# Kernel optimization log

Hardware: AMD Instinct MI355X
Metric: run time of the kernel (lower is better)

Reference implementation:

```python
import jax, jax.numpy as jnp
import numpy as np

C = 256  # channels
B, H, W = 16, 64, 64


def _conv1x1(x, w, b):
    # x: [B,Cin,H,W], w: [Cout,Cin], b: [Cout] -> [B,Cout,H,W]
    return jnp.einsum('bchw,oc->bohw', x, w) + b[None, :, None, None]


def _axis_attn(x, wq, bq, wf, bf, axis):
    # axis: -1 for 'W', -2 for 'H'
    qkv = _conv1x1(x, wq, bq)                      # [B,1+2C,H,W]
    query = qkv[:, :1]                             # [B,1,H,W]
    key = qkv[:, 1:1 + C]                          # [B,C,H,W]
    value = qkv[:, 1 + C:]                         # [B,C,H,W]
    scores = jax.nn.softmax(query, axis=axis)      # softmax over spatial axis
    context = jnp.sum(key * scores, axis=axis, keepdims=True)  # [B,C,H,1] or [B,C,1,W]
    gate = jax.nn.sigmoid(value)
    out = x + gate * context                       # broadcast over reduced axis
    return _conv1x1(out, wf, bf)


def setup_inputs() -> dict:
    key = jax.random.key(0)
    ks = jax.random.split(key, 5)
    s_qkv = 1.0 / np.sqrt(C)
    s_fus = 1.0 / np.sqrt(C)
    return {
        'x': jax.random.normal(ks[0], (B, C, H, W), dtype=jnp.float32),
        'qkvW_w': jax.random.normal(ks[1], (1 + 2 * C, C), dtype=jnp.float32) * s_qkv,
        'qkvW_b': jnp.zeros((1 + 2 * C,), dtype=jnp.float32),
        'qkvH_w': jax.random.normal(ks[2], (1 + 2 * C, C), dtype=jnp.float32) * s_qkv,
        'qkvH_b': jnp.zeros((1 + 2 * C,), dtype=jnp.float32),
        'fusW_w': jax.random.normal(ks[3], (C, C), dtype=jnp.float32) * s_fus,
        'fusW_b': jnp.zeros((C,), dtype=jnp.float32),
        'fusH_w': jax.random.normal(ks[4], (C, C), dtype=jnp.float32) * s_fus,
        'fusH_b': jnp.zeros((C,), dtype=jnp.float32),
    }


def reference(x, qkvW_w, qkvW_b, qkvH_w, qkvH_b, fusW_w, fusW_b, fusH_w, fusH_b):
    x_w = _axis_attn(x, qkvW_w, qkvW_b, fusW_w, fusW_b, axis=-1)
    x_h = _axis_attn(x_w, qkvH_w, qkvH_b, fusH_w, fusH_b, axis=-2)
    return x_h
```

## Files before the change

kernel.cpp:

```cpp
#include <hip/hip_runtime.h>

typedef unsigned short u16;
typedef unsigned int u32;
typedef __attribute__((ext_vector_type(8))) short bf16x8;
typedef __attribute__((ext_vector_type(4))) float f32x4;

__device__ __forceinline__ u16 f2bf(float f) {
    u32 u = __builtin_bit_cast(u32, f);
    u += 0x7FFFu + ((u >> 16) & 1u);
    return (u16)(u >> 16);
}
__device__ __forceinline__ float bf2f(u16 s) {
    u32 u = ((u32)s) << 16;
    return __builtin_bit_cast(float, u);
}
__device__ __forceinline__ float sigm(float x) {
    return 1.0f / (1.0f + __expf(-x));
}
__device__ __forceinline__ void gload16(const u16* g, u16* l) {
    __builtin_amdgcn_global_load_lds(
        (const __attribute__((address_space(1))) void*)g,
        (__attribute__((address_space(3))) void*)l, 16, 0, 0);
}

__global__ __launch_bounds__(256) void transpose_in(const float* __restrict__ x,
                                                    u16* __restrict__ xp) {
    __shared__ float tile[64][65];
    int bid = blockIdx.x;
    int ct = bid & 3, h = (bid >> 2) & 63, b = bid >> 8;
    int t = threadIdx.x;
    int tr = t >> 4, tc = t & 15;
    const float* src = x + (((size_t)(b * 256 + ct * 64) * 64 + h) * 64);
#pragma unroll
    for (int i = 0; i < 4; ++i) {
        int c = tr + i * 16;
        float4 v = *(const float4*)(src + (size_t)c * 4096 + tc * 4);
        tile[c][tc * 4 + 0] = v.x;
        tile[c][tc * 4 + 1] = v.y;
        tile[c][tc * 4 + 2] = v.z;
        tile[c][tc * 4 + 3] = v.w;
    }
    __syncthreads();
    u16* dst = xp + ((size_t)((b * 64 + h) * 64)) * 256 + ct * 64;
#pragma unroll
    for (int i = 0; i < 4; ++i) {
        int w = tr + i * 16;
        ushort4 o;
        o.x = f2bf(tile[tc * 4 + 0][w]);
        o.y = f2bf(tile[tc * 4 + 1][w]);
        o.z = f2bf(tile[tc * 4 + 2][w]);
        o.w = f2bf(tile[tc * 4 + 3][w]);
        *(ushort4*)(dst + (size_t)w * 256 + tc * 4) = o;
    }
}

__global__ __launch_bounds__(256) void prep_w(const float* __restrict__ qw,
                                              const float* __restrict__ qb,
                                              const float* __restrict__ fw,
                                              const float* __restrict__ fb,
                                              float* __restrict__ wq0,
                                              u16* __restrict__ wkv,
                                              float* __restrict__ bkv,
                                              u16* __restrict__ wf,
                                              float* __restrict__ bff) {
    int i = blockIdx.x * 256 + threadIdx.x;
    if (i < 513 * 256) {
        int o = i >> 8, c = i & 255;
        float v = qw[i];
        if (o == 0) wq0[c] = v;
        else        wkv[(size_t)(o - 1) * 256 + c] = f2bf(v);
    }
    if (i < 65536) wf[i] = f2bf(fw[i]);
    if (i < 512)   bkv[i] = qb[i + 1];
    if (i < 256)   bff[i] = fb[i];
}

__global__ __launch_bounds__(256) void ctx_gate(const u16* __restrict__ Xin,
                                                const float* __restrict__ wq0,
                                                const u16* __restrict__ key,
                                                const u16* __restrict__ val,
                                                u16* __restrict__ G, int axis) {
    __shared__ float ql[64];
    __shared__ float sc[64];
    __shared__ alignas(16) float ctxs[256];
    int l = blockIdx.x, t = threadIdx.x;
    int b = l >> 6, lw = l & 63;
    auto pj = [&](int j) {
        return axis ? (b * 4096 + j * 64 + lw) : (l * 64 + j);
    };
    {
        int j = t >> 2, g = t & 3;
        const u16* xr = Xin + (size_t)pj(j) * 256 + g * 64;
        const float* wp = wq0 + g * 64;
        float a0 = 0.f, a1 = 0.f;
#pragma unroll
        for (int i = 0; i < 8; ++i) {
            bf16x8 v = *(const bf16x8*)(xr + i * 8);
#pragma unroll
            for (int jj = 0; jj < 8; ++jj) {
                float p = bf2f((u16)v[jj]) * wp[i * 8 + jj];
                if (jj & 1) a1 += p; else a0 += p;
            }
        }
        float a = a0 + a1;
        a += __shfl_xor(a, 1);
        a += __shfl_xor(a, 2);
        if (g == 0) ql[j] = a;
    }
    __syncthreads();
    if (t < 64) {
        float qv = ql[t];
        float m = qv;
#pragma unroll
        for (int off = 32; off > 0; off >>= 1) m = fmaxf(m, __shfl_xor(m, off));
        float e = __expf(qv - m);
        float s = e;
#pragma unroll
        for (int off = 32; off > 0; off >>= 1) s += __shfl_xor(s, off);
        sc[t] = e / s;
    }
    __syncthreads();
    {
        float a0 = 0.f, a1 = 0.f;
#pragma unroll 4
        for (int j2 = 0; j2 < 64; j2 += 2) {
            a0 += bf2f(key[(size_t)pj(j2) * 256 + t]) * sc[j2];
            a1 += bf2f(key[(size_t)pj(j2 + 1) * 256 + t]) * sc[j2 + 1];
        }
        ctxs[t] = a0 + a1;
    }
    __syncthreads();
    {
        int c0 = (t & 31) * 8;
        float cf[8];
        *(float4*)cf = *(const float4*)&ctxs[c0];
        *(float4*)(cf + 4) = *(const float4*)&ctxs[c0 + 4];
#pragma unroll
        for (int it = 0; it < 8; ++it) {
            int j3 = it * 8 + (t >> 5);
            size_t base = (size_t)pj(j3) * 256 + c0;
            bf16x8 xv = *(const bf16x8*)(Xin + base);
            bf16x8 vv = *(const bf16x8*)(val + base);
            u16 o[8];
#pragma unroll
            for (int jj = 0; jj < 8; ++jj)
                o[jj] = f2bf(bf2f((u16)xv[jj]) +
                             sigm(bf2f((u16)vv[jj])) * cf[jj]);
            *(bf16x8*)(G + base) = *(bf16x8*)o;
        }
    }
}

template <int MODE>
__global__ __launch_bounds__(256, 2) void gemm_k(
    const u16* __restrict__ A, const u16* __restrict__ Bw,
    const float* __restrict__ bias,
    u16* __restrict__ keyOut, u16* __restrict__ valOut,
    float* __restrict__ fOut) {
    int h = blockIdx.x;
    int xcd = h & 7, slot = h >> 3;
    int otile, ptile;
    if (MODE == 0) { otile = slot & 3; ptile = xcd * 64 + (slot >> 2); }
    else           { otile = slot & 1; ptile = xcd * 64 + (slot >> 1); }
    __shared__ alignas(16) u16 Asm[128 * 64];
    __shared__ alignas(16) u16 Bsm[128 * 64];
    int p0 = ptile * 128, o0 = otile * 128;
    int t = threadIdx.x, lane = t & 63, wv = t >> 6;
    int wm = (wv >> 1) * 64, wn = (wv & 1) * 64;
    int l7 = lane & 7;
    int srcoff = (lane >> 3) * 256 + (((lane & 7) ^ (lane >> 3)) * 8);
    int arow = lane & 15, kgrp = lane >> 4;
    f32x4 zero = {0.f, 0.f, 0.f, 0.f};
    f32x4 acc[4][4];
#pragma unroll
    for (int i = 0; i < 4; ++i)
#pragma unroll
        for (int jj = 0; jj < 4; ++jj) acc[i][jj] = zero;

    for (int k0 = 0; k0 < 256; k0 += 64) {
        __syncthreads();
#pragma unroll
        for (int it = 0; it < 4; ++it) {
            int r0 = it * 32 + wv * 8;
            gload16(A + (size_t)(p0 + r0) * 256 + k0 + srcoff, &Asm[r0 * 64]);
            gload16(Bw + (size_t)(o0 + r0) * 256 + k0 + srcoff, &Bsm[r0 * 64]);
        }
        __syncthreads();
#pragma unroll
        for (int kk = 0; kk < 64; kk += 32) {
            int soff = (((kk >> 3) + kgrp) ^ l7) << 3;
            bf16x8 af[4], bfv[4];
#pragma unroll
            for (int mi = 0; mi < 4; ++mi)
                af[mi] = *(const bf16x8*)&Asm[(wm + mi * 16 + arow) * 64 + soff];
#pragma unroll
            for (int ni = 0; ni < 4; ++ni)
                bfv[ni] = *(const bf16x8*)&Bsm[(wn + ni * 16 + arow) * 64 + soff];
#pragma unroll
            for (int mi = 0; mi < 4; ++mi)
#pragma unroll
                for (int ni = 0; ni < 4; ++ni)
                    acc[mi][ni] = __builtin_amdgcn_mfma_f32_16x16x32_bf16(
                        af[mi], bfv[ni], acc[mi][ni], 0, 0, 0);
        }
    }
#pragma unroll
    for (int mi = 0; mi < 4; ++mi) {
#pragma unroll
        for (int ni = 0; ni < 4; ++ni) {
            int col = o0 + wn + ni * 16 + arow;
            float bv = bias[col];
#pragma unroll
            for (int r = 0; r < 4; ++r) {
                int row = p0 + wm + mi * 16 + ((lane >> 4) << 2) + r;
                float v = acc[mi][ni][r] + bv;
                if (MODE == 0) {
                    if (col < 256) keyOut[(size_t)row * 256 + col] = f2bf(v);
                    else           valOut[(size_t)row * 256 + (col - 256)] = f2bf(v);
                } else if (MODE == 1) {
                    keyOut[(size_t)row * 256 + col] = f2bf(v);
                } else {
                    fOut[((size_t)((row >> 12) * 256 + col)) * 4096 + (row & 4095)] = v;
                }
            }
        }
    }
}

extern "C" void kernel_launch(void* const* d_in, const int* in_sizes, int n_in,
                              void* d_out, int out_size, void* d_ws, size_t ws_size,
                              hipStream_t stream) {
    const float* x   = (const float*)d_in[0];
    const float* qWw = (const float*)d_in[1];
    const float* qWb = (const float*)d_in[2];
    const float* qHw = (const float*)d_in[3];
    const float* qHb = (const float*)d_in[4];
    const float* fWw = (const float*)d_in[5];
    const float* fWb = (const float*)d_in[6];
    const float* fHw = (const float*)d_in[7];
    const float* fHb = (const float*)d_in[8];
    float* out = (float*)d_out;

    char* ws = (char*)d_ws;
    size_t off = 0;
    auto carve = [&](size_t bytes) -> void* {
        off = (off + 255) & ~(size_t)255;
        void* p = ws + off;
        off += bytes;
        return p;
    };
    const size_t P = 65536;
    u16*   xp  = (u16*)carve(P * 256 * 2);
    u16*   kb  = (u16*)carve(P * 256 * 2);
    u16*   vb  = (u16*)carve(P * 256 * 2);
    float* wq01 = (float*)carve(256 * 4);
    u16*   wkv1 = (u16*)carve(512 * 256 * 2);
    float* bkv1 = (float*)carve(512 * 4);
    u16*   wf1  = (u16*)carve(65536 * 2);
    float* bf1  = (float*)carve(256 * 4);
    float* wq02 = (float*)carve(256 * 4);
    u16*   wkv2 = (u16*)carve(512 * 256 * 2);
    float* bkv2 = (float*)carve(512 * 4);
    u16*   wf2  = (u16*)carve(65536 * 2);
    float* bf2  = (float*)carve(256 * 4);

    prep_w<<<513, 256, 0, stream>>>(qWw, qWb, fWw, fWb, wq01, wkv1, bkv1, wf1, bf1);
    prep_w<<<513, 256, 0, stream>>>(qHw, qHb, fHw, fHb, wq02, wkv2, bkv2, wf2, bf2);
    transpose_in<<<4096, 256, 0, stream>>>(x, xp);

    gemm_k<0><<<2048, 256, 0, stream>>>(xp, wkv1, bkv1, kb, vb, nullptr);
    ctx_gate<<<1024, 256, 0, stream>>>(xp, wq01, kb, vb, kb, 0);
    gemm_k<1><<<1024, 256, 0, stream>>>(kb, wf1, bf1, vb, nullptr, nullptr);
    gemm_k<0><<<2048, 256, 0, stream>>>(vb, wkv2, bkv2, kb, xp, nullptr);
    ctx_gate<<<1024, 256, 0, stream>>>(vb, wq02, kb, xp, kb, 1);
    gemm_k<2><<<1024, 256, 0, stream>>>(kb, wf2, bf2, nullptr, nullptr, out);
    (void)in_sizes; (void)n_in; (void)out_size; (void)ws_size;
}
```

Before: 176.8 us.

## Fuse key/value GEMM with softmax context and gating into one kernel

Replaces the separate key/value projection GEMM and the ctx_gate kernel with a single qkv_attn kernel. Each block holds 128 pixel rows (two attention lines) of the input in LDS, computes the query and softmax, then runs the key GEMM and reduces it straight into the context without writing key to memory. It then runs the value GEMM and applies sigmoid gating with the residual in the epilogue. This removes the round trip of key and value tensors through global memory and two launches, in exchange for 128KB of LDS per block, which allows only one block per CU, and a strided row layout for the H axis.

```diff
diff --git a/kernel.cpp b/kernel.cpp
--- a/kernel.cpp
+++ b/kernel.cpp
@@ -75,40 +75,50 @@
     if (i < 256)   bff[i] = fb[i];
 }
 
-__global__ __launch_bounds__(256) void ctx_gate(const u16* __restrict__ Xin,
-                                                const float* __restrict__ wq0,
-                                                const u16* __restrict__ key,
-                                                const u16* __restrict__ val,
-                                                u16* __restrict__ G, int axis) {
-    __shared__ float ql[64];
-    __shared__ float sc[64];
-    __shared__ alignas(16) float ctxs[256];
-    int l = blockIdx.x, t = threadIdx.x;
-    int b = l >> 6, lw = l & 63;
-    auto pj = [&](int j) {
-        return axis ? (b * 4096 + j * 64 + lw) : (l * 64 + j);
+template <int AXIS>
+__global__ __launch_bounds__(512, 2) void qkv_attn(
+    const u16* __restrict__ A, const u16* __restrict__ Bw,
+    const float* __restrict__ bkv, const float* __restrict__ wq0,
+    u16* __restrict__ G) {
+    __shared__ alignas(16) u16 Asm[128 * 256];
+    __shared__ alignas(16) u16 Bsm[128 * 256];
+    __shared__ float ql[128];
+    __shared__ float sc[128];
+    __shared__ float ctxs[2][256];
+    int t = threadIdx.x, lane = t & 63, wv = t >> 6;
+    int beta = blockIdx.x;
+    auto prow = [&](int r) -> size_t {
+        if (AXIS == 0) return (size_t)beta * 128 + r;
+        else           return (size_t)(beta >> 5) * 4096 + (size_t)(r & 63) * 64 +
+                              ((beta & 31) * 2) + (r >> 6);
     };
     {
-        int j = t >> 2, g = t & 3;
-        const u16* xr = Xin + (size_t)pj(j) * 256 + g * 64;
+        int r5 = t >> 5, c5 = t & 31;
+#pragma unroll
+        for (int i = 0; i < 8; ++i) {
+            int row = i * 16 + r5;
+            int slot = c5 ^ (row & 7);
+            gload16(A + prow(row) * 256 + slot * 8, &Asm[(i * 16 + wv * 2) * 256]);
+        }
+    }
+    __syncthreads();
+    {
+        int row = t >> 2, g = t & 3;
         const float* wp = wq0 + g * 64;
-        float a0 = 0.f, a1 = 0.f;
-#pragma unroll
-        for (int i = 0; i < 8; ++i) {
-            bf16x8 v = *(const bf16x8*)(xr + i * 8);
-#pragma unroll
-            for (int jj = 0; jj < 8; ++jj) {
-                float p = bf2f((u16)v[jj]) * wp[i * 8 + jj];
-                if (jj & 1) a1 += p; else a0 += p;
-            }
-        }
-        float a = a0 + a1;
+        float a = 0.f;
+#pragma unroll
+        for (int cc = 0; cc < 8; ++cc) {
+            int slot = (g * 8 + cc) ^ (row & 7);
+            bf16x8 v = *(const bf16x8*)&Asm[row * 256 + slot * 8];
+#pragma unroll
+            for (int j = 0; j < 8; ++j) a += bf2f((u16)v[j]) * wp[cc * 8 + j];
+        }
         a += __shfl_xor(a, 1);
         a += __shfl_xor(a, 2);
-        if (g == 0) ql[j] = a;
+        if (g == 0) ql[row] = a;
     }
     __syncthreads();
-    if (t < 64) {
+    if (t < 128) {
         float qv = ql[t];
         float m = qv;
 #pragma unroll
@@ -119,34 +129,80 @@
         for (int off = 32; off > 0; off >>= 1) s += __shfl_xor(s, off);
         sc[t] = e / s;
     }
-    __syncthreads();
-    {
-        float a0 = 0.f, a1 = 0.f;
-#pragma unroll 4
-        for (int j2 = 0; j2 < 64; j2 += 2) {
-            a0 += bf2f(key[(size_t)pj(j2) * 256 + t]) * sc[j2];
-            a1 += bf2f(key[(size_t)pj(j2 + 1) * 256 + t]) * sc[j2 + 1];
-        }
-        ctxs[t] = a0 + a1;
-    }
-    __syncthreads();
-    {
-        int c0 = (t & 31) * 8;
-        float cf[8];
-        *(float4*)cf = *(const float4*)&ctxs[c0];
-        *(float4*)(cf + 4) = *(const float4*)&ctxs[c0 + 4];
-#pragma unroll
-        for (int it = 0; it < 8; ++it) {
-            int j3 = it * 8 + (t >> 5);
-            size_t base = (size_t)pj(j3) * 256 + c0;
-            bf16x8 xv = *(const bf16x8*)(Xin + base);
-            bf16x8 vv = *(const bf16x8*)(val + base);
-            u16 o[8];
-#pragma unroll
-            for (int jj = 0; jj < 8; ++jj)
-                o[jj] = f2bf(bf2f((u16)xv[jj]) +
-                             sigm(bf2f((u16)vv[jj])) * cf[jj]);
-            *(bf16x8*)(G + base) = *(bf16x8*)o;
+    int wm = (wv & 1) * 64, wn = (wv >> 1) * 32;
+    int arow = lane & 15, kgrp = lane >> 4, l7 = lane & 7;
+    int line = wv & 1;
+    for (int ot = 0; ot < 4; ++ot) {
+        __syncthreads();
+        {
+            int r5 = t >> 5, c5 = t & 31;
+#pragma unroll
+            for (int i = 0; i < 8; ++i) {
+                int row = i * 16 + r5;
+                int slot = c5 ^ (row & 7);
+                gload16(Bw + (size_t)(ot * 128 + row) * 256 + slot * 8,
+                        &Bsm[(i * 16 + wv * 2) * 256]);
+            }
+        }
+        __syncthreads();
+        f32x4 zero = {0.f, 0.f, 0.f, 0.f};
+        f32x4 acc[4][2];
+#pragma unroll
+        for (int mi = 0; mi < 4; ++mi) {
+            acc[mi][0] = zero;
+            acc[mi][1] = zero;
+        }
+#pragma unroll
+        for (int ks = 0; ks < 8; ++ks) {
+            int soff = ((ks * 4 + kgrp) ^ l7) * 8;
+            bf16x8 af[4], bf[2];
+#pragma unroll
+            for (int mi = 0; mi < 4; ++mi)
+                af[mi] = *(const bf16x8*)&Asm[(wm + mi * 16 + arow) * 256 + soff];
+#pragma unroll
+            for (int ni = 0; ni < 2; ++ni)
+                bf[ni] = *(const bf16x8*)&Bsm[(wn + ni * 16 + arow) * 256 + soff];
+#pragma unroll
+            for (int mi = 0; mi < 4; ++mi)
+#pragma unroll
+                for (int ni = 0; ni < 2; ++ni)
+                    acc[mi][ni] = __builtin_amdgcn_mfma_f32_16x16x32_bf16(
+                        af[mi], bf[ni], acc[mi][ni], 0, 0, 0);
+        }
+        if (ot < 2) {
+#pragma unroll
+            for (int ni = 0; ni < 2; ++ni) {
+                int col = ot * 128 + wn + ni * 16 + arow;
+                float part = 0.f;
+#pragma unroll
+                for (int mi = 0; mi < 4; ++mi) {
+                    int rbase = wm + mi * 16 + kgrp * 4;
+#pragma unroll
+                    for (int r = 0; r < 4; ++r)
+                        part += acc[mi][ni][r] * sc[rbase + r];
+                }
+                part += __shfl_xor(part, 16);
+                part += __shfl_xor(part, 32);
+                if (lane < 16) ctxs[line][col] = part + bkv[col];
+            }
+        } else {
+#pragma unroll
+            for (int ni = 0; ni < 2; ++ni) {
+                int c = (ot - 2) * 128 + wn + ni * 16 + arow;
+                float bv = bkv[256 + c];
+                float cx = ctxs[line][c];
+#pragma unroll
+                for (int mi = 0; mi < 4; ++mi) {
+#pragma unroll
+                    for (int r = 0; r < 4; ++r) {
+                        int row = wm + mi * 16 + kgrp * 4 + r;
+                        float v = acc[mi][ni][r] + bv;
+                        int slot = (c >> 3) ^ (row & 7);
+                        float xv = bf2f(Asm[row * 256 + slot * 8 + (c & 7)]);
+                        G[prow(row) * 256 + c] = f2bf(xv + sigm(v) * cx);
+                    }
+                }
+            }
         }
     }
 }
@@ -155,13 +211,10 @@
 __global__ __launch_bounds__(256, 2) void gemm_k(
     const u16* __restrict__ A, const u16* __restrict__ Bw,
     const float* __restrict__ bias,
-    u16* __restrict__ keyOut, u16* __restrict__ valOut,
-    float* __restrict__ fOut) {
+    u16* __restrict__ bOut, float* __restrict__ fOut) {
     int h = blockIdx.x;
     int xcd = h & 7, slot = h >> 3;
-    int otile, ptile;
-    if (MODE == 0) { otile = slot & 3; ptile = xcd * 64 + (slot >> 2); }
-    else           { otile = slot & 1; ptile = xcd * 64 + (slot >> 1); }
+    int otile = slot & 1, ptile = xcd * 64 + (slot >> 1);
     __shared__ alignas(16) u16 Asm[128 * 64];
     __shared__ alignas(16) u16 Bsm[128 * 64];
     int p0 = ptile * 128, o0 = otile * 128;
@@ -214,11 +267,8 @@
             for (int r = 0; r < 4; ++r) {
                 int row = p0 + wm + mi * 16 + ((lane >> 4) << 2) + r;
                 float v = acc[mi][ni][r] + bv;
-                if (MODE == 0) {
-                    if (col < 256) keyOut[(size_t)row * 256 + col] = f2bf(v);
-                    else           valOut[(size_t)row * 256 + (col - 256)] = f2bf(v);
-                } else if (MODE == 1) {
-                    keyOut[(size_t)row * 256 + col] = f2bf(v);
+                if (MODE == 1) {
+                    bOut[(size_t)row * 256 + col] = f2bf(v);
                 } else {
                     fOut[((size_t)((row >> 12) * 256 + col)) * 4096 + (row & 4095)] = v;
                 }
@@ -268,11 +318,9 @@
     prep_w<<<513, 256, 0, stream>>>(qHw, qHb, fHw, fHb, wq02, wkv2, bkv2, wf2, bf2);
     transpose_in<<<4096, 256, 0, stream>>>(x, xp);
 
-    gemm_k<0><<<2048, 256, 0, stream>>>(xp, wkv1, bkv1, kb, vb, nullptr);
-    ctx_gate<<<1024, 256, 0, stream>>>(xp, wq01, kb, vb, kb, 0);
-    gemm_k<1><<<1024, 256, 0, stream>>>(kb, wf1, bf1, vb, nullptr, nullptr);
-    gemm_k<0><<<2048, 256, 0, stream>>>(vb, wkv2, bkv2, kb, xp, nullptr);
-    ctx_gate<<<1024, 256, 0, stream>>>(vb, wq02, kb, xp, kb, 1);
-    gemm_k<2><<<1024, 256, 0, stream>>>(kb, wf2, bf2, nullptr, nullptr, out);
+    qkv_attn<0><<<512, 512, 0, stream>>>(xp, wkv1, bkv1, wq01, kb);
+    gemm_k<1><<<1024, 256, 0, stream>>>(kb, wf1, bf1, vb, nullptr);
+    qkv_attn<1><<<512, 512, 0, stream>>>(vb, wkv2, bkv2, wq02, kb);
+    gemm_k<2><<<1024, 256, 0, stream>>>(kb, wf2, bf2, nullptr, out);
     (void)in_sizes; (void)n_in; (void)out_size; (void)ws_size;
 }
```

Result: faster. 160.6 us (-9.2%).
